# Kernel optimization log

Hardware: AMD Instinct MI355X
Metric: run time of the kernel (lower is better)

The kernel has to match this reference:

```python
import jax, jax.numpy as jnp
import numpy as np

NUM_LEVELS = 16
LEVEL_DIM = 2
BASE_RES = 16
PER_LEVEL_SCALE = 2.0
LOG2_HASHMAP = 19
INPUT_DIM = 3
N_POINTS = 2_000_000
B = 262144


def _compute_offsets():
    offsets = []
    off = 0
    max_params = 2 ** LOG2_HASHMAP
    for i in range(NUM_LEVELS):
        res = int(np.ceil(BASE_RES * PER_LEVEL_SCALE ** i))
        p = min(max_params, (res + 1) ** INPUT_DIM)  # align_corners=False -> res+1 verts per axis
        p = int(np.ceil(p / 8) * 8)
        offsets.append(off)
        off += p
    offsets.append(off)
    return offsets

OFFSETS = _compute_offsets()
TOTAL_PARAMS = OFFSETS[-1]  # 7131240
PRIMES = (1, 2654435761, 805459861)  # instant-ngp fast_hash primes for D=3
CORNER_BITS = np.array([[(c >> d) & 1 for d in range(3)] for c in range(8)], dtype=np.int32)  # [8,3]


def _build_table(embeddings, fs_embeddings, scatter_index):
    # scatter_add point embeddings (and counts) into grid vertices, then blend
    sums = jnp.zeros((TOTAL_PARAMS, LEVEL_DIM), embeddings.dtype).at[scatter_index].add(embeddings)
    counts = jnp.zeros((TOTAL_PARAMS,), embeddings.dtype).at[scatter_index].add(1.0)
    sel = jnp.minimum(counts, 1.0)[:, None]
    num = jnp.maximum(counts, 1.0)[:, None]
    return (sums / num) * sel + fs_embeddings * (1.0 - sel)


def _grid_encode(x, table):
    # x: [B,3] in [0,1]; table: [TOTAL_PARAMS, C]. Multi-res hash grid, linear interp,
    # align_corners=False (matches torch-ngp grid_encode CUDA kernel).
    S = np.log2(PER_LEVEL_SCALE)
    bits_i = jnp.asarray(CORNER_BITS)                 # [8,3] int
    bits_f = jnp.asarray(CORNER_BITS, dtype=x.dtype)  # [8,3] float
    outs = []
    for level in range(NUM_LEVELS):
        scale = np.exp2(level * S) * BASE_RES - 1.0
        resolution = int(np.ceil(scale)) + 1
        hashmap_size = OFFSETS[level + 1] - OFFSETS[level]
        pos = x * scale + 0.5  # align_corners=False offset
        pos_grid = jnp.floor(pos)
        frac = pos - pos_grid                                  # [B,3]
        corner = pos_grid.astype(jnp.int32)[:, None, :] + bits_i  # [B,8,3]
        stride = (resolution + 1) ** 3
        if stride > hashmap_size:
            # hashed level: xor of per-dim prime products, uint32 wraparound
            cu = corner.astype(jnp.uint32)
            idx = (cu[..., 0] * jnp.uint32(PRIMES[0])) ^ \
                  (cu[..., 1] * jnp.uint32(PRIMES[1])) ^ \
                  (cu[..., 2] * jnp.uint32(PRIMES[2]))
            idx = (idx % jnp.uint32(hashmap_size)).astype(jnp.int32)
        else:
            # dense level: row-major index with stride (res+1)
            r1 = resolution + 1
            idx = (corner[..., 0] + corner[..., 1] * r1 + corner[..., 2] * (r1 * r1)) % hashmap_size
        vals = table[idx + OFFSETS[level]]  # [B,8,C] gather
        w = jnp.prod(jnp.where(bits_f > 0, frac[:, None, :], 1.0 - frac[:, None, :]), axis=-1)  # [B,8]
        outs.append(jnp.einsum('bk,bkc->bc', w, vals))
    return jnp.concatenate(outs, axis=-1)  # [B, L*C]


def setup_inputs() -> dict:
    key = jax.random.key(0)
    k1, k2, k3, k4 = jax.random.split(key, 4)
    std = 1e-4  # reset_parameters() uniform(-1e-4, 1e-4)
    inputs = jax.random.uniform(k1, (B, 3), jnp.float32, minval=-1.0, maxval=1.0)
    embeddings = jax.random.uniform(k2, (N_POINTS, LEVEL_DIM), jnp.float32, minval=-std, maxval=std)
    fs_embeddings = jax.random.uniform(k3, (TOTAL_PARAMS, LEVEL_DIM), jnp.float32, minval=-std, maxval=std)
    scatter_index = jax.random.randint(k4, (N_POINTS,), 0, TOTAL_PARAMS, dtype=jnp.int32)
    return {"inputs": inputs, "embeddings": embeddings, "fs_embeddings": fs_embeddings,
            "scatter_index": scatter_index, "bound": 1}


def reference(inputs, embeddings, fs_embeddings, scatter_index, bound):
    table = _build_table(embeddings, fs_embeddings, scatter_index)
    x = (inputs + bound) / (2.0 * bound)  # map to [0,1]
    return _grid_encode(x, table)  # [B, NUM_LEVELS*LEVEL_DIM]
```

## Files before the change

kernel.cpp:

```cpp
#include <hip/hip_runtime.h>

#define TOTAL_PARAMS 7131240
#define NLEVELS 16
#define NB 262144
#define HASH_MASK 0x7FFFF

#define SF 5.24288e9f
#define CF 1e-4f

__constant__ int c_off[NLEVELS] = {
    0, 4920, 40864, 315496, 839784, 1364072, 1888360, 2412648,
    2936936, 3461224, 3985512, 4509800, 5034088, 5558376, 6082664, 6606952};

typedef float vfloat2 __attribute__((ext_vector_type(2)));
typedef float vfloat4 __attribute__((ext_vector_type(4)));

__global__ __launch_bounds__(256) void scatter_kernel(
    const vfloat2* __restrict__ emb, const int* __restrict__ sidx,
    double* __restrict__ accum, int n) {
    int i = blockIdx.x * 256 + threadIdx.x;
    if (i >= n) return;
    int idx = __builtin_nontemporal_load(&sidx[i]);
    vfloat2 e = __builtin_nontemporal_load(&emb[i]);
    unsigned qx = __float2uint_rn((e.x + CF) * SF);
    unsigned qy = __float2uint_rn((e.y + CF) * SF);
    unsigned long long p =
        (1ULL << 48) | ((unsigned long long)qx << 24) | (unsigned long long)qy;
    unsafeAtomicAdd(&accum[idx], (double)p);
}

__device__ __forceinline__ unsigned short f2bf(float f) {
    unsigned u = __builtin_bit_cast(unsigned, f);
    return (unsigned short)((u + 0x7FFFu + ((u >> 16) & 1u)) >> 16);
}

__global__ __launch_bounds__(256) void finalize_kernel(
    const double* __restrict__ accum, const vfloat2* __restrict__ fs,
    unsigned* __restrict__ table_bf, int n) {
    int i = blockIdx.x * 256 + threadIdx.x;
    if (i >= n) return;
    double v = __builtin_nontemporal_load(&accum[i]);
    unsigned long long u = (unsigned long long)v;
    unsigned cnt = (unsigned)(u >> 48);
    float rx, ry;
    if (cnt == 0) {
        vfloat2 f = __builtin_nontemporal_load(&fs[i]);
        rx = f.x;
        ry = f.y;
    } else {
        double qxs = (double)((u >> 24) & 0xFFFFFFULL);
        double qys = (double)(u & 0xFFFFFFULL);
        double inv = 1.0 / ((double)SF * (double)cnt);
        rx = (float)(qxs * inv - (double)CF);
        ry = (float)(qys * inv - (double)CF);
    }
    table_bf[i] = (unsigned)f2bf(rx) | ((unsigned)f2bf(ry) << 16);
}

__device__ __forceinline__ vfloat2 level_interp(
    float px, float py, float pz, int l, const unsigned* __restrict__ table_bf) {
#pragma clang fp contract(off)
    int res = 16 << l;
    float scale = (float)(res - 1);
    float posx = px * scale + 0.5f;
    float posy = py * scale + 0.5f;
    float posz = pz * scale + 0.5f;
    float gx = floorf(posx), gy = floorf(posy), gz = floorf(posz);
    float fx = posx - gx, fy = posy - gy, fz = posz - gz;
    int ix = (int)gx, iy = (int)gy, iz = (int)gz;

    const unsigned* tb = table_bf + c_off[l];
    bool dense = (l < 3);
    int r1 = res + 1;
    int r1sq = r1 * r1;

    float ax = 0.0f, ay = 0.0f;
#pragma unroll
    for (int c = 0; c < 8; ++c) {
        int bx = c & 1, by = (c >> 1) & 1, bz = (c >> 2) & 1;
        int cx = ix + bx, cy = iy + by, cz = iz + bz;
        unsigned idx;
        if (dense) {
            idx = (unsigned)(cx + cy * r1 + cz * r1sq);
        } else {
            idx = ((unsigned)cx * 1u) ^ ((unsigned)cy * 2654435761u) ^
                  ((unsigned)cz * 805459861u);
            idx &= HASH_MASK;
        }
        unsigned v = tb[idx];
        float vx = __builtin_bit_cast(float, v << 16);
        float vy = __builtin_bit_cast(float, v & 0xFFFF0000u);
        float wx = bx ? fx : (1.0f - fx);
        float wy = by ? fy : (1.0f - fy);
        float wz = bz ? fz : (1.0f - fz);
        float w = (wx * wy) * wz;
        ax += w * vx;
        ay += w * vy;
    }
    vfloat2 r;
    r.x = ax;
    r.y = ay;
    return r;
}

__global__ __launch_bounds__(256) void encode_hash_kernel(
    const float* __restrict__ x, const int* __restrict__ bound_p,
    const unsigned* __restrict__ table_bf, vfloat2* __restrict__ lm) {
#pragma clang fp contract(off)
    int l = 15 - (blockIdx.x >> 10);
    int b = ((blockIdx.x & 1023) << 8) + threadIdx.x;

    float bound = (float)bound_p[0];
    float denom = 2.0f * bound;
    float px = (x[b * 3 + 0] + bound) / denom;
    float py = (x[b * 3 + 1] + bound) / denom;
    float pz = (x[b * 3 + 2] + bound) / denom;

    vfloat2 o = level_interp(px, py, pz, l, table_bf);
    __builtin_nontemporal_store(o, &lm[(l - 3) * NB + b]);
}

__global__ __launch_bounds__(256) void finish_kernel(
    const float* __restrict__ x, const int* __restrict__ bound_p,
    const unsigned* __restrict__ table_bf, const vfloat2* __restrict__ lm,
    float* __restrict__ out) {
#pragma clang fp contract(off)
    int b = blockIdx.x * 256 + threadIdx.x;

    float bound = (float)bound_p[0];
    float denom = 2.0f * bound;
    float px = (x[b * 3 + 0] + bound) / denom;
    float py = (x[b * 3 + 1] + bound) / denom;
    float pz = (x[b * 3 + 2] + bound) / denom;

    float row[2 * NLEVELS];

#pragma unroll
    for (int lev = 0; lev < 13; ++lev) {
        vfloat2 v = lm[lev * NB + b];
        row[2 * (lev + 3)] = v.x;
        row[2 * (lev + 3) + 1] = v.y;
    }
#pragma unroll
    for (int l = 0; l < 3; ++l) {
        vfloat2 o = level_interp(px, py, pz, l, table_bf);
        row[2 * l] = o.x;
        row[2 * l + 1] = o.y;
    }

    vfloat4* op = (vfloat4*)&out[b * 32];
#pragma unroll
    for (int k = 0; k < 8; ++k) {
        vfloat4 o;
        o.x = row[4 * k + 0];
        o.y = row[4 * k + 1];
        o.z = row[4 * k + 2];
        o.w = row[4 * k + 3];
        op[k] = o;
    }
}

extern "C" void kernel_launch(void* const* d_in, const int* in_sizes, int n_in,
                              void* d_out, int out_size, void* d_ws, size_t ws_size,
                              hipStream_t stream) {
    const float* x     = (const float*)d_in[0];
    const float* emb   = (const float*)d_in[1];
    const float* fs    = (const float*)d_in[2];
    const int*   sidx  = (const int*)d_in[3];
    const int*   bound = (const int*)d_in[4];

    double*   accum    = (double*)d_ws;
    unsigned* table_bf = (unsigned*)(accum + TOTAL_PARAMS);
    vfloat2*  lm       = (vfloat2*)d_ws;

    int npts = in_sizes[3];
    int B = in_sizes[0] / 3;

    (void)hipMemsetAsync(d_ws, 0, (size_t)TOTAL_PARAMS * sizeof(double), stream);

    scatter_kernel<<<(npts + 255) / 256, 256, 0, stream>>>(
        (const vfloat2*)emb, sidx, accum, npts);

    finalize_kernel<<<(TOTAL_PARAMS + 255) / 256, 256, 0, stream>>>(
        accum, (const vfloat2*)fs, table_bf, TOTAL_PARAMS);

    encode_hash_kernel<<<13 * (B / 256), 256, 0, stream>>>(
        x, bound, table_bf, lm);

    finish_kernel<<<B / 256, 256, 0, stream>>>(
        x, bound, table_bf, lm, (float*)d_out);
}
```

Before: 343.5 us.

## Pack scatter accumulators into 32-bit ints and pair-load interpolation corners

```diff
diff --git a/kernel.cpp b/kernel.cpp
--- a/kernel.cpp
+++ b/kernel.cpp
@@ -5,7 +5,7 @@
 #define NB 262144
 #define HASH_MASK 0x7FFFF
 
-#define SF 5.24288e9f
+#define SF2 5115000.0f
 #define CF 1e-4f
 
 __constant__ int c_off[NLEVELS] = {
@@ -14,19 +14,33 @@
 
 typedef float vfloat2 __attribute__((ext_vector_type(2)));
 typedef float vfloat4 __attribute__((ext_vector_type(4)));
+typedef unsigned vuint2 __attribute__((ext_vector_type(2)));
+typedef int vint2 __attribute__((ext_vector_type(2)));
 
 __global__ __launch_bounds__(256) void scatter_kernel(
-    const vfloat2* __restrict__ emb, const int* __restrict__ sidx,
-    double* __restrict__ accum, int n) {
+    const vfloat4* __restrict__ emb2, const vint2* __restrict__ sidx2,
+    unsigned* __restrict__ accum, int n) {
     int i = blockIdx.x * 256 + threadIdx.x;
-    if (i >= n) return;
-    int idx = __builtin_nontemporal_load(&sidx[i]);
-    vfloat2 e = __builtin_nontemporal_load(&emb[i]);
-    unsigned qx = __float2uint_rn((e.x + CF) * SF);
-    unsigned qy = __float2uint_rn((e.y + CF) * SF);
-    unsigned long long p =
-        (1ULL << 48) | ((unsigned long long)qx << 24) | (unsigned long long)qy;
-    unsafeAtomicAdd(&accum[idx], (double)p);
+    int base = i * 2;
+    if (base >= n) return;
+    if (base + 1 < n) {
+        vint2 idx = __builtin_nontemporal_load(&sidx2[i]);
+        vfloat4 e = __builtin_nontemporal_load(&emb2[i]);
+        unsigned qx0 = __float2uint_rn((e.x + CF) * SF2);
+        unsigned qy0 = __float2uint_rn((e.y + CF) * SF2);
+        unsigned qx1 = __float2uint_rn((e.z + CF) * SF2);
+        unsigned qy1 = __float2uint_rn((e.w + CF) * SF2);
+        atomicAdd(&accum[idx.x], (1u << 28) | (qx0 << 14) | qy0);
+        atomicAdd(&accum[idx.y], (1u << 28) | (qx1 << 14) | qy1);
+    } else {
+        const int* sidx = (const int*)sidx2;
+        const vfloat2* emb = (const vfloat2*)emb2;
+        int idx = sidx[base];
+        vfloat2 e = emb[base];
+        unsigned qx = __float2uint_rn((e.x + CF) * SF2);
+        unsigned qy = __float2uint_rn((e.y + CF) * SF2);
+        atomicAdd(&accum[idx], (1u << 28) | (qx << 14) | qy);
+    }
 }
 
 __device__ __forceinline__ unsigned short f2bf(float f) {
@@ -35,31 +49,37 @@
 }
 
 __global__ __launch_bounds__(256) void finalize_kernel(
-    const double* __restrict__ accum, const vfloat2* __restrict__ fs,
-    unsigned* __restrict__ table_bf, int n) {
+    const unsigned* __restrict__ accum, const vfloat4* __restrict__ fs2,
+    unsigned long long* __restrict__ table2, int npairs) {
     int i = blockIdx.x * 256 + threadIdx.x;
-    if (i >= n) return;
-    double v = __builtin_nontemporal_load(&accum[i]);
-    unsigned long long u = (unsigned long long)v;
-    unsigned cnt = (unsigned)(u >> 48);
-    float rx, ry;
-    if (cnt == 0) {
-        vfloat2 f = __builtin_nontemporal_load(&fs[i]);
-        rx = f.x;
-        ry = f.y;
-    } else {
-        double qxs = (double)((u >> 24) & 0xFFFFFFULL);
-        double qys = (double)(u & 0xFFFFFFULL);
-        double inv = 1.0 / ((double)SF * (double)cnt);
-        rx = (float)(qxs * inv - (double)CF);
-        ry = (float)(qys * inv - (double)CF);
-    }
-    table_bf[i] = (unsigned)f2bf(rx) | ((unsigned)f2bf(ry) << 16);
-}
-
+    if (i >= npairs) return;
+    vuint2 a = __builtin_nontemporal_load((const vuint2*)(accum + 2 * i));
+    unsigned c0 = a.x >> 28, c1 = a.y >> 28;
+    vfloat4 f = {0.0f, 0.0f, 0.0f, 0.0f};
+    if ((c0 == 0u) | (c1 == 0u)) f = __builtin_nontemporal_load(&fs2[i]);
+    float rx0, ry0, rx1, ry1;
+    if (c0 == 0u) {
+        rx0 = f.x; ry0 = f.y;
+    } else {
+        float inv = 1.0f / ((float)c0 * SF2);
+        rx0 = (float)((a.x >> 14) & 0x3FFFu) * inv - CF;
+        ry0 = (float)(a.x & 0x3FFFu) * inv - CF;
+    }
+    if (c1 == 0u) {
+        rx1 = f.z; ry1 = f.w;
+    } else {
+        float inv = 1.0f / ((float)c1 * SF2);
+        rx1 = (float)((a.y >> 14) & 0x3FFFu) * inv - CF;
+        ry1 = (float)(a.y & 0x3FFFu) * inv - CF;
+    }
+    unsigned lo = (unsigned)f2bf(rx0) | ((unsigned)f2bf(ry0) << 16);
+    unsigned hi = (unsigned)f2bf(rx1) | ((unsigned)f2bf(ry1) << 16);
+    table2[i] = (unsigned long long)lo | ((unsigned long long)hi << 32);
+}
+
+template <bool DENSE>
 __device__ __forceinline__ vfloat2 level_interp(
     float px, float py, float pz, int l, const unsigned* __restrict__ table_bf) {
-#pragma clang fp contract(off)
     int res = 16 << l;
     float scale = (float)(res - 1);
     float posx = px * scale + 0.5f;
@@ -69,33 +89,71 @@
     float fx = posx - gx, fy = posy - gy, fz = posz - gz;
     int ix = (int)gx, iy = (int)gy, iz = (int)gz;
 
-    const unsigned* tb = table_bf + c_off[l];
-    bool dense = (l < 3);
-    int r1 = res + 1;
-    int r1sq = r1 * r1;
-
+    const unsigned* __restrict__ tb = table_bf + c_off[l];
+
+    unsigned tyz[4];
+    if (DENSE) {
+        unsigned r1u = (unsigned)(res + 1);
+        unsigned r1sq = r1u * r1u;
+        unsigned ty0 = (unsigned)iy * r1u;
+        unsigned tz0 = (unsigned)iz * r1sq;
+        tyz[0] = ty0 + tz0;
+        tyz[1] = ty0 + r1u + tz0;
+        tyz[2] = ty0 + tz0 + r1sq;
+        tyz[3] = ty0 + r1u + tz0 + r1sq;
+    } else {
+        unsigned ty0 = (unsigned)iy * 2654435761u;
+        unsigned ty1 = ty0 + 2654435761u;
+        unsigned tz0 = (unsigned)iz * 805459861u;
+        unsigned tz1 = tz0 + 805459861u;
+        tyz[0] = ty0 ^ tz0;
+        tyz[1] = ty1 ^ tz0;
+        tyz[2] = ty0 ^ tz1;
+        tyz[3] = ty1 ^ tz1;
+    }
+
+    unsigned i0[4], i1[4];
+    vuint2 P[4];
+#pragma unroll
+    for (int c = 0; c < 4; ++c) {
+        if (DENSE) {
+            i0[c] = tyz[c] + (unsigned)ix;
+            i1[c] = i0[c] + 1u;
+        } else {
+            i0[c] = ((unsigned)ix ^ tyz[c]) & HASH_MASK;
+            i1[c] = (((unsigned)ix + 1u) ^ tyz[c]) & HASH_MASK;
+        }
+        P[c] = *(const vuint2*)(tb + (i0[c] & ~1u));
+    }
+    unsigned vX[4];
+#pragma unroll
+    for (int c = 0; c < 4; ++c) {
+        vX[c] = 0u;
+        if (i1[c] != (i0[c] ^ 1u)) vX[c] = tb[i1[c]];
+    }
+
+    float wy0 = 1.0f - fy, wz0 = 1.0f - fz;
+    float wyzv[4];
+    wyzv[0] = wy0 * wz0;
+    wyzv[1] = fy * wz0;
+    wyzv[2] = wy0 * fz;
+    wyzv[3] = fy * fz;
+    float wx0 = 1.0f - fx;
     float ax = 0.0f, ay = 0.0f;
 #pragma unroll
-    for (int c = 0; c < 8; ++c) {
-        int bx = c & 1, by = (c >> 1) & 1, bz = (c >> 2) & 1;
-        int cx = ix + bx, cy = iy + by, cz = iz + bz;
-        unsigned idx;
-        if (dense) {
-            idx = (unsigned)(cx + cy * r1 + cz * r1sq);
-        } else {
-            idx = ((unsigned)cx * 1u) ^ ((unsigned)cy * 2654435761u) ^
-                  ((unsigned)cz * 805459861u);
-            idx &= HASH_MASK;
-        }
-        unsigned v = tb[idx];
-        float vx = __builtin_bit_cast(float, v << 16);
-        float vy = __builtin_bit_cast(float, v & 0xFFFF0000u);
-        float wx = bx ? fx : (1.0f - fx);
-        float wy = by ? fy : (1.0f - fy);
-        float wz = bz ? fz : (1.0f - fz);
-        float w = (wx * wy) * wz;
-        ax += w * vx;
-        ay += w * vy;
+    for (int c = 0; c < 4; ++c) {
+        unsigned lo = P[c].x, hi = P[c].y;
+        bool odd = (i0[c] & 1u) != 0u;
+        unsigned v0 = odd ? hi : lo;
+        unsigned vo = odd ? lo : hi;
+        unsigned v1 = (i1[c] == (i0[c] ^ 1u)) ? vo : vX[c];
+        float v0x = __builtin_bit_cast(float, v0 << 16);
+        float v0y = __builtin_bit_cast(float, v0 & 0xFFFF0000u);
+        float v1x = __builtin_bit_cast(float, v1 << 16);
+        float v1y = __builtin_bit_cast(float, v1 & 0xFFFF0000u);
+        float w = wyzv[c];
+        ax += w * (wx0 * v0x + fx * v1x);
+        ay += w * (wx0 * v0y + fx * v1y);
     }
     vfloat2 r;
     r.x = ax;
@@ -106,7 +164,6 @@
 __global__ __launch_bounds__(256) void encode_hash_kernel(
     const float* __restrict__ x, const int* __restrict__ bound_p,
     const unsigned* __restrict__ table_bf, vfloat2* __restrict__ lm) {
-#pragma clang fp contract(off)
     int l = 15 - (blockIdx.x >> 10);
     int b = ((blockIdx.x & 1023) << 8) + threadIdx.x;
 
@@ -116,7 +173,7 @@
     float py = (x[b * 3 + 1] + bound) / denom;
     float pz = (x[b * 3 + 2] + bound) / denom;
 
-    vfloat2 o = level_interp(px, py, pz, l, table_bf);
+    vfloat2 o = level_interp<false>(px, py, pz, l, table_bf);
     __builtin_nontemporal_store(o, &lm[(l - 3) * NB + b]);
 }
 
@@ -124,7 +181,6 @@
     const float* __restrict__ x, const int* __restrict__ bound_p,
     const unsigned* __restrict__ table_bf, const vfloat2* __restrict__ lm,
     float* __restrict__ out) {
-#pragma clang fp contract(off)
     int b = blockIdx.x * 256 + threadIdx.x;
 
     float bound = (float)bound_p[0];
@@ -143,7 +199,7 @@
     }
 #pragma unroll
     for (int l = 0; l < 3; ++l) {
-        vfloat2 o = level_interp(px, py, pz, l, table_bf);
+        vfloat2 o = level_interp<true>(px, py, pz, l, table_bf);
         row[2 * l] = o.x;
         row[2 * l + 1] = o.y;
     }
@@ -169,20 +225,22 @@
     const int*   sidx  = (const int*)d_in[3];
     const int*   bound = (const int*)d_in[4];
 
-    double*   accum    = (double*)d_ws;
-    unsigned* table_bf = (unsigned*)(accum + TOTAL_PARAMS);
+    unsigned* accum    = (unsigned*)d_ws;
+    unsigned* table_bf = accum + TOTAL_PARAMS;
     vfloat2*  lm       = (vfloat2*)d_ws;
 
     int npts = in_sizes[3];
     int B = in_sizes[0] / 3;
 
-    (void)hipMemsetAsync(d_ws, 0, (size_t)TOTAL_PARAMS * sizeof(double), stream);
-
-    scatter_kernel<<<(npts + 255) / 256, 256, 0, stream>>>(
-        (const vfloat2*)emb, sidx, accum, npts);
-
-    finalize_kernel<<<(TOTAL_PARAMS + 255) / 256, 256, 0, stream>>>(
-        accum, (const vfloat2*)fs, table_bf, TOTAL_PARAMS);
+    (void)hipMemsetAsync(d_ws, 0, (size_t)TOTAL_PARAMS * sizeof(unsigned), stream);
+
+    int npair_pts = (npts + 1) / 2;
+    scatter_kernel<<<(npair_pts + 255) / 256, 256, 0, stream>>>(
+        (const vfloat4*)emb, (const vint2*)sidx, accum, npts);
+
+    int npairs = TOTAL_PARAMS / 2;
+    finalize_kernel<<<(npairs + 255) / 256, 256, 0, stream>>>(
+        accum, (const vfloat4*)fs, (unsigned long long*)table_bf, npairs);
 
     encode_hash_kernel<<<13 * (B / 256), 256, 0, stream>>>(
         x, bound, table_bf, lm);
```

After: 330.1 us. -3.9%, faster.
